# Kernel optimization log

Measured on AMD Instinct MI355X. Metric: run time of the kernel, lower is better.

## Reference

```python
import jax, jax.numpy as jnp
import numpy as np

B, N, F_IN, F_HID, F_EMB, H, L_DIM = 8, 1024, 128, 128, 128, 8, 2


def _xavier(key, shape, fan_in, fan_out):
    lim = np.sqrt(6.0 / (fan_in + fan_out))
    return jax.random.uniform(key, shape, jnp.float32, -lim, lim)


def setup_inputs() -> dict:
    key = jax.random.key(0)
    ks = jax.random.split(key, 16)
    x = jax.random.normal(ks[0], (B, N, F_IN), jnp.float32)
    # sparse 0/1 adjacency with self loops (avoids fully-masked softmax rows)
    adj = (jax.random.uniform(ks[1], (B, N, N)) < 0.05).astype(jnp.float32)
    adj = jnp.maximum(adj, jnp.eye(N, dtype=jnp.float32)[None])
    def gat_params(k, f_in, f_out):
        k1, k2, k3 = jax.random.split(k, 3)
        return (_xavier(k1, (H, f_in, f_out), f_in, f_out),
                _xavier(k2, (H, f_out, 1), f_out, 1),
                _xavier(k3, (H, f_out, 1), f_out, 1),
                jnp.zeros((f_out,), jnp.float32))
    w1, as1, ad1, b1 = gat_params(ks[2], F_IN, F_HID)
    w2, as2, ad2, b2 = gat_params(ks[3], F_HID, F_HID)
    w3, as3, ad3, b3 = gat_params(ks[4], F_HID, F_EMB)
    pred_in = F_HID * 2 + F_EMB  # hidden*(num_layers-1)+embedding, concat=True
    pw = _xavier(ks[5], (pred_in, L_DIM), pred_in, L_DIM)
    pb = jnp.zeros((L_DIM,), jnp.float32)
    return {"x": x, "adj": adj,
            "w1": w1, "as1": as1, "ad1": ad1, "b1": b1,
            "w2": w2, "as2": as2, "ad2": ad2, "b2": b2,
            "w3": w3, "as3": as3, "ad3": ad3, "b3": b3,
            "pw": pw, "pb": pb}


def gat_layer(h, adj, w, a_src, a_dst, bias):
    # h: [B,N,f_in] -> h_prime: [B,H,N,f_out]
    hp = jnp.einsum('bnf,hfo->bhno', h, w)
    t = jnp.tanh(hp)
    s = jnp.einsum('bhno,hoi->bhni', t, a_src)[..., 0]  # [B,H,N]
    d = jnp.einsum('bhno,hoi->bhni', t, a_dst)[..., 0]  # [B,H,N]
    scores = s[:, :, :, None] + d[:, :, None, :]        # [B,H,N,N]
    scores = jnp.where(scores >= 0, scores, 0.2 * scores)  # LeakyReLU(0.2)
    scores = jnp.where(adj[:, None, :, :] > 0, scores, -jnp.inf)
    attn = jax.nn.softmax(scores, axis=-1)  # dropout disabled (eval mode)
    out = jnp.einsum('bhnm,bhmo->bhno', attn, hp) + bias
    return out.mean(axis=1)  # merge heads -> [B,N,f_out]


def reference(x, adj, w1, as1, ad1, b1, w2, as2, ad2, b2, w3, as3, ad3, b3, pw, pb):
    x1 = jax.nn.relu(gat_layer(x, adj, w1, as1, ad1, b1))
    x2 = jax.nn.relu(gat_layer(x1, adj, w2, as2, ad2, b2))
    x3 = gat_layer(x2, adj, w3, as3, ad3, b3)
    x_all = jnp.concatenate([x1, x2, x3], axis=2)  # [B,N,pred_in]
    pooled = jnp.max(x_all, axis=1)                # max over nodes -> [B,pred_in]
    return pooled @ pw + pb                        # [B,label_dim]
```

## Files before the change

kernel.cpp:

```cpp
#include <hip/hip_runtime.h>
#include <hip/hip_fp16.h>

#define BB 8
#define NN 1024
#define FF 128
#define HH 8

typedef _Float16 f16;
typedef f16  f16x8 __attribute__((ext_vector_type(8)));
typedef f16  f16x4 __attribute__((ext_vector_type(4)));
typedef float f32x4 __attribute__((ext_vector_type(4)));

#define L2E 1.44269504f

__global__ void k_pre(const float* __restrict__ x, f16* __restrict__ x16a,
                      const float* __restrict__ w1, const float* __restrict__ w2,
                      const float* __restrict__ w3, f16* __restrict__ wB,
                      const float* __restrict__ adj, unsigned* __restrict__ am){
  int bid = blockIdx.x, t = threadIdx.x;
  if (bid < 512){
    int i = (bid*256 + t)*8;
    float4 a = *(const float4*)(x+i), b = *(const float4*)(x+i+4);
    f16x8 v;
    v[0]=(f16)a.x; v[1]=(f16)a.y; v[2]=(f16)a.z; v[3]=(f16)a.w;
    v[4]=(f16)b.x; v[5]=(f16)b.y; v[6]=(f16)b.z; v[7]=(f16)b.w;
    *(f16x8*)(x16a+i) = v;
  } else if (bid < 704){
    int e = (bid-512)*256 + t;
    int fc = e & 15, c = (e>>4)&127, h = (e>>11)&7, l = e>>14;
    const float* w = (l==0) ? w1 : ((l==1) ? w2 : w3);
    f16x8 v;
    #pragma unroll
    for(int j=0;j<8;j++) v[j] = (f16)w[(h*128 + fc*8 + j)*128 + c];
    *(f16x8*)(wB + (((l*8+h)*16 + fc)*128 + c)*8) = v;
  } else {
    int wv = t >> 6, lane = t & 63;
    int r = (bid-704)*4 + wv;
    const float* row = adj + (long)r*1024;
    for(int g=0; g<16; g++){
      float v = row[g*64 + lane];
      unsigned long long mb = __ballot(v > 0.0f);
      if (lane == 0){
        am[r*32 + 2*g]   = (unsigned)mb;
        am[r*32 + 2*g+1] = (unsigned)(mb >> 32);
      }
    }
  }
}

__global__ __launch_bounds__(256,2) void k_hp(
    const f16* __restrict__ xin,
    const f16* __restrict__ wBl,
    const float* __restrict__ asrc, const float* __restrict__ adst,
    f16* __restrict__ hpB,
    float* __restrict__ sarr, float* __restrict__ darr)
{
  __shared__ f16 xs[128*136];
  __shared__ float asl[128], adl[128];
  int t = threadIdx.x;
  int bid = blockIdx.x;
  int h = bid & 7, it = (bid>>3)&7, b = bid>>6;
  int i0 = it*128;
  {
    const f16* src = xin + (long)(b*1024 + i0)*128;
    int fc = t & 15, r0 = t >> 4;
    #pragma unroll
    for(int p=0;p<8;p++){
      int r = r0 + p*16;
      f16x8 v = *(const f16x8*)(src + r*128 + fc*8);
      *(f16x8*)(xs + r*136 + fc*8) = v;
    }
  }
  if (t < 128){ asl[t] = asrc[h*128+t]; adl[t] = adst[h*128+t]; }
  __syncthreads();

  int lane = t & 63, wv = t>>6, wr = wv>>1, wc = wv&1;
  int mq = lane & 15, quad = lane >> 4;
  f32x4 acc[4][4];
  #pragma unroll
  for(int a=0;a<4;a++)
    #pragma unroll
    for(int c=0;c<4;c++) acc[a][c] = (f32x4){0.f,0.f,0.f,0.f};

  const f16* wh = wBl + h*16*128*8;
  #pragma unroll
  for(int ks=0; ks<4; ks++){
    f16x8 af[4], bf[4];
    #pragma unroll
    for(int mt=0; mt<4; mt++)
      af[mt] = *(const f16x8*)(xs + (wr*64 + mt*16 + mq)*136 + ks*32 + quad*8);
    #pragma unroll
    for(int nt=0; nt<4; nt++){
      int c  = wc*64 + nt*16 + mq;
      int fc = ks*4 + quad;
      bf[nt] = *(const f16x8*)(wh + (fc*128 + c)*8);
    }
    #pragma unroll
    for(int mt=0; mt<4; mt++)
      #pragma unroll
      for(int nt=0; nt<4; nt++)
        acc[mt][nt] = __builtin_amdgcn_mfma_f32_16x16x32_f16(af[mt], bf[nt], acc[mt][nt], 0,0,0);
  }
  __syncthreads();
  f16* tt = xs;
  f16* hpb = hpB + (long)(b*8+h)*128*128*8;
  #pragma unroll
  for(int mt=0; mt<4; mt++){
    #pragma unroll
    for(int nt=0; nt<4; nt++){
      int c = wc*64 + nt*16 + mq;
      f16x4 pk;
      #pragma unroll
      for(int rg=0; rg<4; rg++){
        float v = acc[mt][nt][rg];
        pk[rg] = (f16)v;
        int il = wr*64 + mt*16 + quad*4 + rg;
        float e2 = __expf(2.0f*v);
        float th = 1.0f - 2.0f*__builtin_amdgcn_rcpf(e2 + 1.0f);
        tt[il*136 + c] = (f16)th;
      }
      int il0 = wr*64 + mt*16 + quad*4;
      int inode = i0 + il0;
      *(f16x4*)(hpb + ((long)(inode>>3)*128 + c)*8 + (inode&7)) = pk;
    }
  }
  __syncthreads();
  {
    int r = t>>1, hf = t&1;
    float s_p = 0.f, d_p = 0.f;
    #pragma unroll
    for(int q=0;q<8;q++){
      f16x8 tv = *(const f16x8*)(tt + r*136 + hf*64 + q*8);
      #pragma unroll
      for(int j=0;j<8;j++){
        float tvf = (float)tv[j];
        int c = hf*64 + q*8 + j;
        s_p = fmaf(tvf, asl[c], s_p);
        d_p = fmaf(tvf, adl[c], d_p);
      }
    }
    s_p += __shfl_xor(s_p, 1);
    d_p += __shfl_xor(d_p, 1);
    if (hf == 0){
      sarr[(b*8+h)*1024 + i0 + r] = s_p;
      darr[(b*8+h)*1024 + i0 + r] = d_p;
    }
  }
}

__global__ __launch_bounds__(256,4) void k_attn(
    const f16* __restrict__ hpB,
    const float* __restrict__ sarr, const float* __restrict__ darr,
    const unsigned* __restrict__ am,
    f16* __restrict__ part)
{
  __shared__ float ddl[1024];
  __shared__ float wred[4];
  __shared__ float zl[64];
  __shared__ f16 Pl[2][64*72];
  int t = threadIdx.x;
  int bid = blockIdx.x;
  int bh = bid & 63, it = bid >> 6;
  int i0 = it*64;
  int b = bh >> 3;

  int lane = t&63, wv = t>>6;
  int mq = lane&15, quad = lane>>4;
  const f16* hpb = hpB + (long)bh*128*128*8;

  {
    float4 v = *(const float4*)(darr + bh*1024 + t*4);
    float mx = fmaxf(fmaxf(v.x,v.y), fmaxf(v.z,v.w));
    #pragma unroll
    for(int o=1;o<64;o<<=1) mx = fmaxf(mx, __shfl_xor(mx, o));
    if (lane == 0) wred[wv] = mx;
    *(float4*)(ddl + t*4) = make_float4(v.x*L2E, v.y*L2E, v.z*L2E, v.w*L2E);
  }

  int prow = t>>2, pg = t&3;
  float srowl = sarr[bh*1024 + i0 + prow] * L2E;
  const unsigned* amrow = am + ((long)(b*1024 + i0 + prow))*32;
  int wsel = pg >> 1, wsh = (pg&1)*16;

  f16x8 bf[3][4];
  #pragma unroll
  for(int kk=0;kk<2;kk++)
    #pragma unroll
    for(int nt=0;nt<2;nt++){
      int c  = wv*32 + nt*16 + mq;
      bf[0][kk*2+nt] = *(const f16x8*)(hpb + ((long)(kk*4 + quad)*128 + c)*8);
      bf[1][kk*2+nt] = *(const f16x8*)(hpb + ((long)(8 + kk*4 + quad)*128 + c)*8);
    }
  unsigned wcur = amrow[wsel];
  unsigned wnx  = amrow[2 + wsel];

  __syncthreads();
  float Dml = fmaxf(fmaxf(wred[0],wred[1]), fmaxf(wred[2],wred[3])) * L2E;
  float ml = srowl + Dml;
  float mrowl = fmaxf(ml, 0.2f*ml);

  f32x4 acc[4][2];
  #pragma unroll
  for(int a=0;a<4;a++){ acc[a][0] = (f32x4){0.f,0.f,0.f,0.f}; acc[a][1] = (f32x4){0.f,0.f,0.f,0.f}; }
  float zacc = 0.f;
  f16x8 zerov = (f16x8){0,0,0,0,0,0,0,0};

#define PFILL(BUF, WORDSRC, DBASE)                                        \
  {                                                                       \
    f16* myp = Pl[BUF] + prow*72 + pg*16;                                 \
    *(f16x8*)myp = zerov; *(f16x8*)(myp+8) = zerov;                       \
    unsigned word = ((WORDSRC) >> wsh) & 0xffffu;                         \
    const float* dloc = ddl + (DBASE) + pg*16;                            \
    if (word){                                                            \
      int n = __popc(word);                                               \
      unsigned w = word;                                                  \
      int j0 = __builtin_ctz(w); w &= w-1u;                               \
      int j1 = w ? __builtin_ctz(w) : j0; w = w ? (w & (w-1u)) : 0u;      \
      int j2 = w ? __builtin_ctz(w) : j0; w = w ? (w & (w-1u)) : 0u;      \
      int j3 = w ? __builtin_ctz(w) : j0;                                 \
      unsigned wrest = w ? (w & (w-1u)) : 0u;                             \
      float v0 = dloc[j0], v1 = dloc[j1], v2 = dloc[j2], v3 = dloc[j3];   \
      float x0 = srowl+v0, x1 = srowl+v1, x2 = srowl+v2, x3 = srowl+v3;   \
      float e0 = __builtin_amdgcn_exp2f(fmaxf(x0,0.2f*x0) - mrowl);       \
      float e1 = __builtin_amdgcn_exp2f(fmaxf(x1,0.2f*x1) - mrowl);      \
      float e2 = __builtin_amdgcn_exp2f(fmaxf(x2,0.2f*x2) - mrowl);      \
      float e3 = __builtin_amdgcn_exp2f(fmaxf(x3,0.2f*x3) - mrowl);      \
      zacc += e0; myp[j0] = (f16)e0;                                      \
      if (n > 1){ zacc += e1; myp[j1] = (f16)e1; }                        \
      if (n > 2){ zacc += e2; myp[j2] = (f16)e2; }                        \
      if (n > 3){ zacc += e3; myp[j3] = (f16)e3; }                        \
      while (wrest){                                                      \
        int j = __builtin_ctz(wrest); wrest &= wrest-1u;                  \
        float xl = srowl + dloc[j];                                       \
        float e  = __builtin_amdgcn_exp2f(fmaxf(xl,0.2f*xl) - mrowl);     \
        zacc += e; myp[j] = (f16)e;                                       \
      }                                                                   \
    }                                                                     \
  }

  PFILL(0, wcur, 0)
  __syncthreads();

  #pragma unroll
  for(int jt=0; jt<16; jt++){
    if (jt < 14){
      #pragma unroll
      for(int kk=0;kk<2;kk++)
        #pragma unroll
        for(int nt=0;nt<2;nt++){
          int c  = wv*32 + nt*16 + mq;
          int jc = (jt+2)*8 + kk*4 + quad;
          bf[(jt+2)%3][kk*2+nt] = *(const f16x8*)(hpb + ((long)jc*128 + c)*8);
        }
    }
    if (jt < 15){
      unsigned wfut = (jt < 14) ? amrow[(jt+2)*2 + wsel] : 0u;
      PFILL((jt+1)&1, wnx, (jt+1)*64)
      wnx = wfut;
    }
    const f16* Pc = Pl[jt&1];
    #pragma unroll
    for(int kk=0;kk<2;kk++){
      #pragma unroll
      for(int mt=0;mt<4;mt++){
        f16x8 a = *(const f16x8*)(Pc + (mt*16+mq)*72 + kk*32 + quad*8);
        #pragma unroll
        for(int nt=0;nt<2;nt++)
          acc[mt][nt] = __builtin_amdgcn_mfma_f32_16x16x32_f16(a, bf[jt%3][kk*2+nt], acc[mt][nt], 0,0,0);
      }
    }
    __syncthreads();
  }
#undef PFILL

  zacc += __shfl_xor(zacc, 1);
  zacc += __shfl_xor(zacc, 2);
  if (pg == 0) zl[prow] = zacc;
  __syncthreads();

  f16* Ps = (f16*)Pl;
  #pragma unroll
  for(int mt=0;mt<4;mt++){
    #pragma unroll
    for(int rg=0;rg<4;rg++){
      int il = mt*16 + quad*4 + rg;
      float zi = 0.125f * __builtin_amdgcn_rcpf(zl[il]);
      #pragma unroll
      for(int nt=0;nt<2;nt++){
        int c = wv*32 + nt*16 + mq;
        Ps[il*136 + c] = (f16)(acc[mt][nt][rg] * zi);
      }
    }
  }
  __syncthreads();
  {
    int r = t>>2, g = t&3;
    f16* dst = part + ((long)bh*1024 + i0 + r)*128 + g*32;
    const f16* srcp = Ps + r*136 + g*32;
    *(f16x8*)(dst)    = *(const f16x8*)(srcp);
    *(f16x8*)(dst+8)  = *(const f16x8*)(srcp+8);
    *(f16x8*)(dst+16) = *(const f16x8*)(srcp+16);
    *(f16x8*)(dst+24) = *(const f16x8*)(srcp+24);
  }
}

__global__ void k_fin(const f16* __restrict__ part, const float* __restrict__ bias,
                      f16* __restrict__ x16, float* __restrict__ pmax, int do_relu){
  __shared__ float pm[16][128];
  int t = threadIdx.x;
  int idx = blockIdx.x*256 + t;
  int c8 = idx & 15, n = (idx>>4)&1023, b = idx>>14;
  float s[8];
  #pragma unroll
  for(int j=0;j<8;j++) s[j] = 0.f;
  #pragma unroll
  for(int h=0;h<8;h++){
    int bh = b*8 + h;
    f16x8 p0 = *(const f16x8*)(part + ((long)bh*1024 + n)*128 + c8*8);
    #pragma unroll
    for(int j=0;j<8;j++) s[j] += (float)p0[j];
  }
  f16x8 h8;
  float ov[8];
  #pragma unroll
  for(int j=0;j<8;j++){
    float v = s[j] + bias[c8*8 + j];
    if (do_relu) v = fmaxf(v, 0.f);
    ov[j] = v;
    h8[j] = (f16)v;
  }
  if (x16) *(f16x8*)(x16 + ((long)(b*1024+n))*128 + c8*8) = h8;
  #pragma unroll
  for(int j=0;j<8;j++) pm[n&15][c8*8+j] = ov[j];
  __syncthreads();
  if (t < 128){
    float m = pm[0][t];
    #pragma unroll
    for(int r=1;r<16;r++) m = fmaxf(m, pm[r][t]);
    pmax[blockIdx.x*128 + t] = m;
  }
}

__global__ void k_pool2(const float* __restrict__ pmax, const float* __restrict__ pw,
                        const float* __restrict__ pb, float* __restrict__ out){
  __shared__ float ph[2][384];
  __shared__ float pl[384];
  int b = blockIdx.x, t = threadIdx.x;
  int c = t & 127, half = t >> 7;
  #pragma unroll
  for(int l=0;l<3;l++){
    const float* p = pmax + l*65536 + b*8192 + half*32*128 + c;
    float m = -3.4e38f;
    #pragma unroll 8
    for(int kk=0;kk<32;kk++) m = fmaxf(m, p[kk*128]);
    ph[half][l*128 + c] = m;
  }
  __syncthreads();
  for(int f = t; f < 384; f += 256) pl[f] = fmaxf(ph[0][f], ph[1][f]);
  __syncthreads();
  if (t < 64){
    float a0 = 0.f, a1 = 0.f;
    #pragma unroll
    for(int k=0;k<6;k++){
      int f = t + 64*k;
      float v = pl[f];
      a0 = fmaf(v, pw[f*2],   a0);
      a1 = fmaf(v, pw[f*2+1], a1);
    }
    #pragma unroll
    for(int o=1;o<64;o<<=1){ a0 += __shfl_xor(a0,o); a1 += __shfl_xor(a1,o); }
    if (t == 0){ out[b*2] = a0 + pb[0]; out[b*2+1] = a1 + pb[1]; }
  }
}

extern "C" void kernel_launch(void* const* d_in, const int* in_sizes, int n_in,
                              void* d_out, int out_size, void* d_ws, size_t ws_size,
                              hipStream_t stream) {
  const float* x   = (const float*)d_in[0];
  const float* adj = (const float*)d_in[1];
  const float* w1  = (const float*)d_in[2];
  const float* as1 = (const float*)d_in[3];
  const float* ad1 = (const float*)d_in[4];
  const float* b1  = (const float*)d_in[5];
  const float* w2  = (const float*)d_in[6];
  const float* as2 = (const float*)d_in[7];
  const float* ad2 = (const float*)d_in[8];
  const float* b2  = (const float*)d_in[9];
  const float* w3  = (const float*)d_in[10];
  const float* as3 = (const float*)d_in[11];
  const float* ad3 = (const float*)d_in[12];
  const float* b3  = (const float*)d_in[13];
  const float* pw  = (const float*)d_in[14];
  const float* pb  = (const float*)d_in[15];

  char* ws = (char*)d_ws;
  f16*      x16a = (f16*)ws;                 ws += (size_t)1048576*2;
  f16*      x16b = (f16*)ws;                 ws += (size_t)1048576*2;
  f16*      wB   = (f16*)ws;                 ws += (size_t)393216*2;
  unsigned* am   = (unsigned*)ws;            ws += (size_t)8*1024*32*4;
  f16*      hpB  = (f16*)ws;                 ws += (size_t)8*8*1024*128*2;
  float*    sarr = (float*)ws;               ws += (size_t)65536*4;
  float*    darr = (float*)ws;               ws += (size_t)65536*4;
  f16*      part = (f16*)ws;                 ws += (size_t)64*1024*128*2;
  float*    pmax = (float*)ws;               ws += (size_t)3*512*128*4;

  k_pre<<<2752, 256, 0, stream>>>(x, x16a, w1, w2, w3, wB, adj, am);

  k_hp  <<<512, 256, 0, stream>>>(x16a, wB,            as1, ad1, hpB, sarr, darr);
  k_attn<<<1024,256, 0, stream>>>(hpB, sarr, darr, am, part);
  k_fin <<<512, 256, 0, stream>>>(part, b1, x16b, pmax,           1);
  k_hp  <<<512, 256, 0, stream>>>(x16b, wB + 131072,   as2, ad2, hpB, sarr, darr);
  k_attn<<<1024,256, 0, stream>>>(hpB, sarr, darr, am, part);
  k_fin <<<512, 256, 0, stream>>>(part, b2, x16a, pmax + 65536,   1);
  k_hp  <<<512, 256, 0, stream>>>(x16a, wB + 262144,   as3, ad3, hpB, sarr, darr);
  k_attn<<<1024,256, 0, stream>>>(hpB, sarr, darr, am, part);
  k_fin <<<512, 256, 0, stream>>>(part, b3, nullptr, pmax + 131072, 0);

  k_pool2<<<8, 256, 0, stream>>>(pmax, pw, pb, (float*)d_out);
}
```

Baseline: 249.9 us.

## Fuse head-merge finalize into next layer's projection kernel

Adds k_hpf, which sums per-head partial attention outputs, adds bias, applies ReLU and writes the result into shared memory as the input tile of the next layer's MFMA projection. Block h==0 also records the per-tile column max for pooling. This removes two k_fin launches and the round trip of the intermediate f16 activations through global memory. In exchange, each of the 8 head blocks for a tile redundantly reads and reduces all 8 head partials, which multiplies reads of the part buffer by eight.

```diff
diff --git a/kernel.cpp b/kernel.cpp
--- a/kernel.cpp
+++ b/kernel.cpp
@@ -73,6 +73,135 @@
   }
   if (t < 128){ asl[t] = asrc[h*128+t]; adl[t] = adst[h*128+t]; }
   __syncthreads();
+
+  int lane = t & 63, wv = t>>6, wr = wv>>1, wc = wv&1;
+  int mq = lane & 15, quad = lane >> 4;
+  f32x4 acc[4][4];
+  #pragma unroll
+  for(int a=0;a<4;a++)
+    #pragma unroll
+    for(int c=0;c<4;c++) acc[a][c] = (f32x4){0.f,0.f,0.f,0.f};
+
+  const f16* wh = wBl + h*16*128*8;
+  #pragma unroll
+  for(int ks=0; ks<4; ks++){
+    f16x8 af[4], bf[4];
+    #pragma unroll
+    for(int mt=0; mt<4; mt++)
+      af[mt] = *(const f16x8*)(xs + (wr*64 + mt*16 + mq)*136 + ks*32 + quad*8);
+    #pragma unroll
+    for(int nt=0; nt<4; nt++){
+      int c  = wc*64 + nt*16 + mq;
+      int fc = ks*4 + quad;
+      bf[nt] = *(const f16x8*)(wh + (fc*128 + c)*8);
+    }
+    #pragma unroll
+    for(int mt=0; mt<4; mt++)
+      #pragma unroll
+      for(int nt=0; nt<4; nt++)
+        acc[mt][nt] = __builtin_amdgcn_mfma_f32_16x16x32_f16(af[mt], bf[nt], acc[mt][nt], 0,0,0);
+  }
+  __syncthreads();
+  f16* tt = xs;
+  f16* hpb = hpB + (long)(b*8+h)*128*128*8;
+  #pragma unroll
+  for(int mt=0; mt<4; mt++){
+    #pragma unroll
+    for(int nt=0; nt<4; nt++){
+      int c = wc*64 + nt*16 + mq;
+      f16x4 pk;
+      #pragma unroll
+      for(int rg=0; rg<4; rg++){
+        float v = acc[mt][nt][rg];
+        pk[rg] = (f16)v;
+        int il = wr*64 + mt*16 + quad*4 + rg;
+        float e2 = __expf(2.0f*v);
+        float th = 1.0f - 2.0f*__builtin_amdgcn_rcpf(e2 + 1.0f);
+        tt[il*136 + c] = (f16)th;
+      }
+      int il0 = wr*64 + mt*16 + quad*4;
+      int inode = i0 + il0;
+      *(f16x4*)(hpb + ((long)(inode>>3)*128 + c)*8 + (inode&7)) = pk;
+    }
+  }
+  __syncthreads();
+  {
+    int r = t>>1, hf = t&1;
+    float s_p = 0.f, d_p = 0.f;
+    #pragma unroll
+    for(int q=0;q<8;q++){
+      f16x8 tv = *(const f16x8*)(tt + r*136 + hf*64 + q*8);
+      #pragma unroll
+      for(int j=0;j<8;j++){
+        float tvf = (float)tv[j];
+        int c = hf*64 + q*8 + j;
+        s_p = fmaf(tvf, asl[c], s_p);
+        d_p = fmaf(tvf, adl[c], d_p);
+      }
+    }
+    s_p += __shfl_xor(s_p, 1);
+    d_p += __shfl_xor(d_p, 1);
+    if (hf == 0){
+      sarr[(b*8+h)*1024 + i0 + r] = s_p;
+      darr[(b*8+h)*1024 + i0 + r] = d_p;
+    }
+  }
+}
+
+__global__ __launch_bounds__(256,2) void k_hpf(
+    const f16* __restrict__ part,
+    const float* __restrict__ biasp,
+    const f16* __restrict__ wBl,
+    const float* __restrict__ asrc, const float* __restrict__ adst,
+    f16* __restrict__ hpB, float* __restrict__ sarr, float* __restrict__ darr,
+    float* __restrict__ pmaxl)
+{
+  __shared__ f16 xs[128*136];
+  __shared__ float asl[128], adl[128];
+  __shared__ float pmf[16][128];
+  int t = threadIdx.x;
+  int bid = blockIdx.x;
+  int h = bid & 7, it = (bid>>3)&7, b = bid>>6;
+  int i0 = it*128;
+  {
+    int c8 = t & 15, rr = t >> 4;
+    float bl[8], vmax[8];
+    #pragma unroll
+    for(int j=0;j<8;j++){ bl[j] = biasp[c8*8+j]; vmax[j] = -3.4e38f; }
+    #pragma unroll
+    for(int p=0;p<8;p++){
+      int row = rr + p*16;
+      float s[8];
+      #pragma unroll
+      for(int j=0;j<8;j++) s[j] = bl[j];
+      #pragma unroll
+      for(int hh=0;hh<8;hh++){
+        f16x8 pv = *(const f16x8*)(part + ((long)(b*8+hh)*1024 + i0 + row)*128 + c8*8);
+        #pragma unroll
+        for(int j=0;j<8;j++) s[j] += (float)pv[j];
+      }
+      f16x8 o;
+      #pragma unroll
+      for(int j=0;j<8;j++){
+        float v = fmaxf(s[j], 0.f);
+        vmax[j] = fmaxf(vmax[j], v);
+        o[j] = (f16)v;
+      }
+      *(f16x8*)(xs + row*136 + c8*8) = o;
+    }
+    if (h == 0){
+      #pragma unroll
+      for(int j=0;j<8;j++) pmf[rr][c8*8+j] = vmax[j];
+    }
+  }
+  if (t < 128){ asl[t] = asrc[h*128+t]; adl[t] = adst[h*128+t]; }
+  __syncthreads();
+  if (h == 0 && t < 128){
+    float m = pmf[0][t];
+    #pragma unroll
+    for(int r=1;r<16;r++) m = fmaxf(m, pmf[r][t]);
+    pmaxl[(b*8+it)*128 + t] = m;
+  }
 
   int lane = t & 63, wv = t>>6, wr = wv>>1, wc = wv&1;
   int mq = lane & 15, quad = lane >> 4;
@@ -341,22 +470,26 @@
   }
 }
 
-__global__ void k_pool2(const float* __restrict__ pmax, const float* __restrict__ pw,
-                        const float* __restrict__ pb, float* __restrict__ out){
-  __shared__ float ph[2][384];
+__global__ void k_pool2(const float* __restrict__ pmax0, const float* __restrict__ pmax1,
+                        const float* __restrict__ pmax2,
+                        const float* __restrict__ pw, const float* __restrict__ pb,
+                        float* __restrict__ out){
   __shared__ float pl[384];
   int b = blockIdx.x, t = threadIdx.x;
-  int c = t & 127, half = t >> 7;
-  #pragma unroll
-  for(int l=0;l<3;l++){
-    const float* p = pmax + l*65536 + b*8192 + half*32*128 + c;
-    float m = -3.4e38f;
-    #pragma unroll 8
-    for(int kk=0;kk<32;kk++) m = fmaxf(m, p[kk*128]);
-    ph[half][l*128 + c] = m;
-  }
-  __syncthreads();
-  for(int f = t; f < 384; f += 256) pl[f] = fmaxf(ph[0][f], ph[1][f]);
+  for(int f = t; f < 384; f += 256){
+    int l = f >> 7, c = f & 127;
+    float mx = -3.4e38f;
+    if (l < 2){
+      const float* p = (l==0 ? pmax0 : pmax1) + b*8*128 + c;
+      #pragma unroll
+      for(int k=0;k<8;k++) mx = fmaxf(mx, p[k*128]);
+    } else {
+      const float* p = pmax2 + b*64*128 + c;
+      #pragma unroll 8
+      for(int k=0;k<64;k++) mx = fmaxf(mx, p[k*128]);
+    }
+    pl[f] = mx;
+  }
   __syncthreads();
   if (t < 64){
     float a0 = 0.f, a1 = 0.f;
@@ -395,26 +528,25 @@
 
   char* ws = (char*)d_ws;
   f16*      x16a = (f16*)ws;                 ws += (size_t)1048576*2;
-  f16*      x16b = (f16*)ws;                 ws += (size_t)1048576*2;
   f16*      wB   = (f16*)ws;                 ws += (size_t)393216*2;
   unsigned* am   = (unsigned*)ws;            ws += (size_t)8*1024*32*4;
   f16*      hpB  = (f16*)ws;                 ws += (size_t)8*8*1024*128*2;
   float*    sarr = (float*)ws;               ws += (size_t)65536*4;
   float*    darr = (float*)ws;               ws += (size_t)65536*4;
   f16*      part = (f16*)ws;                 ws += (size_t)64*1024*128*2;
-  float*    pmax = (float*)ws;               ws += (size_t)3*512*128*4;
+  float*    pmax0= (float*)ws;               ws += (size_t)64*128*4;
+  float*    pmax1= (float*)ws;               ws += (size_t)64*128*4;
+  float*    pmax2= (float*)ws;               ws += (size_t)512*128*4;
 
   k_pre<<<2752, 256, 0, stream>>>(x, x16a, w1, w2, w3, wB, adj, am);
 
   k_hp  <<<512, 256, 0, stream>>>(x16a, wB,            as1, ad1, hpB, sarr, darr);
   k_attn<<<1024,256, 0, stream>>>(hpB, sarr, darr, am, part);
-  k_fin <<<512, 256, 0, stream>>>(part, b1, x16b, pmax,           1);
-  k_hp  <<<512, 256, 0, stream>>>(x16b, wB + 131072,   as2, ad2, hpB, sarr, darr);
+  k_hpf <<<512, 256, 0, stream>>>(part, b1, wB + 131072, as2, ad2, hpB, sarr, darr, pmax0);
   k_attn<<<1024,256, 0, stream>>>(hpB, sarr, darr, am, part);
-  k_fin <<<512, 256, 0, stream>>>(part, b2, x16a, pmax + 65536,   1);
-  k_hp  <<<512, 256, 0, stream>>>(x16a, wB + 262144,   as3, ad3, hpB, sarr, darr);
+  k_hpf <<<512, 256, 0, stream>>>(part, b2, wB + 262144, as3, ad3, hpB, sarr, darr, pmax1);
   k_attn<<<1024,256, 0, stream>>>(hpB, sarr, darr, am, part);
-  k_fin <<<512, 256, 0, stream>>>(part, b3, nullptr, pmax + 131072, 0);
-
-  k_pool2<<<8, 256, 0, stream>>>(pmax, pw, pb, (float*)d_out);
-}
+  k_fin <<<512, 256, 0, stream>>>(part, b3, nullptr, pmax2, 0);
+
+  k_pool2<<<8, 256, 0, stream>>>(pmax0, pmax1, pmax2, pw, pb, (float*)d_out);
+}
```

Measured after the change: 267.8 us. 7.2% more time.
